# Optimization experiments

Hardware: AMD Instinct MI355X
Metric: run time of the kernel (lower is better)

## Reference

```python
import jax, jax.numpy as jnp
import numpy as np

N_NODES = 100000
N_EDGES = 3200000


def gcn_conv(x, src, dst, W, b, n):
    # GCNConv with self-loops and symmetric deg^-1/2 normalization (PyG defaults)
    loop = jnp.arange(n)
    s = jnp.concatenate([src, loop])
    d = jnp.concatenate([dst, loop])
    deg = jax.ops.segment_sum(jnp.ones_like(s, dtype=x.dtype), d, num_segments=n)
    dinv = jnp.where(deg > 0, jax.lax.rsqrt(deg), 0.0)
    norm = dinv[s] * dinv[d]                      # [E+N]
    h = x @ W.T                                   # [N, out]
    msgs = h[s] * norm[:, None]                   # gather + scale
    return jax.ops.segment_sum(msgs, d, num_segments=n) + b


def setup_inputs() -> dict:
    key = jax.random.key(0)
    k = jax.random.split(key, 6)
    x = jax.random.normal(k[0], (N_NODES, 64), dtype=jnp.float32)
    edge_index = jax.random.randint(k[1], (2, N_EDGES), 0, N_NODES, dtype=jnp.int64)
    # glorot-ish init for GCNConv linear weights, zero bias (PyG default bias init is zeros)
    W1 = jax.random.normal(k[2], (32, 64), dtype=jnp.float32) * (1.0 / np.sqrt(64))
    b1 = jnp.zeros((32,), dtype=jnp.float32)
    W2 = jax.random.normal(k[3], (16, 32), dtype=jnp.float32) * (1.0 / np.sqrt(32))
    b2 = jnp.zeros((16,), dtype=jnp.float32)
    return {"x": x, "edge_index": edge_index, "W1": W1, "b1": b1, "W2": W2, "b2": b2}


def reference(x, edge_index, W1, b1, W2, b2):
    n = x.shape[0]
    src, dst = edge_index[0], edge_index[1]
    # encode (eval mode: dropout is identity)
    h = jax.nn.relu(gcn_conv(x, src, dst, W1, b1, n))
    z = gcn_conv(h, src, dst, W2, b2, n)          # [N, 16]
    # decode: edge-wise dot product + sigmoid
    return jax.nn.sigmoid(jnp.sum(z[src] * z[dst], axis=-1))  # [E]
```

## Files before the change

kernel.cpp:

```cpp
#include <hip/hip_runtime.h>
#include <hip/hip_fp16.h>
#include <math.h>

#define NN 100000
#define NE 3200000
#define NB 391
#define NBH 256
#define CH 4096
#define NPART ((NE + CH - 1) / CH)

typedef unsigned long long u64;
typedef _Float16 h2 __attribute__((ext_vector_type(2)));

__device__ inline float2 u2f2(unsigned v) {
    __half2 h = *reinterpret_cast<__half2*>(&v);
    return __half22float2(h);
}

#if __has_builtin(__builtin_amdgcn_fdot2)
__device__ inline float dot2acc(unsigned a, unsigned b, float c) {
    union { unsigned u; h2 h; } ca, cb;
    ca.u = a; cb.u = b;
    return __builtin_amdgcn_fdot2(ca.h, cb.h, c, false);
}
#else
__device__ inline float dot2acc(unsigned a, unsigned b, float c) {
    float2 fa = u2f2(a), fb = u2f2(b);
    return c + fa.x * fb.x + fa.y * fb.y;
}
#endif

__global__ __launch_bounds__(256) void bhist_kernel(const int* __restrict__ dst,
                                                    int* __restrict__ part, int e) {
    __shared__ int h[NB];
    int tid = threadIdx.x;
    for (int i = tid; i < NB; i += 256) h[i] = 0;
    __syncthreads();
    for (int i = blockIdx.x * 256 + tid; i < e; i += NBH * 256)
        atomicAdd(&h[dst[i] >> 8], 1);
    __syncthreads();
    for (int i = tid; i < NB; i += 256)
        part[blockIdx.x * NB + i] = h[i];
}

__global__ __launch_bounds__(512) void bscan_kernel(const int* __restrict__ part,
                                                    int* __restrict__ bhist,
                                                    int* __restrict__ boffs,
                                                    int* __restrict__ cursor) {
    __shared__ int s[512];
    int tid = threadIdx.x;
    int v = 0;
    if (tid < NB) {
#pragma unroll 8
        for (int b = 0; b < NBH; ++b) v += part[b * NB + tid];
        bhist[tid] = v;
    }
    s[tid] = (tid < NB) ? v : 0;
    __syncthreads();
    for (int off = 1; off < 512; off <<= 1) {
        int t = (tid >= off) ? s[tid - off] : 0;
        __syncthreads();
        s[tid] += t;
        __syncthreads();
    }
    if (tid < NB) {
        int ex = s[tid] - v;
        boffs[tid] = ex;
        cursor[tid] = ex;
    }
}

__global__ __launch_bounds__(512) void partition_kernel(
        const int* __restrict__ src, const int* __restrict__ dst,
        int* __restrict__ cursor, int* __restrict__ adj, int e) {
    __shared__ int scnt[NB];
    __shared__ int sbase[NB];
    __shared__ int lexcl[NB];
    __shared__ int cur[NB];
    __shared__ int s[512];
    __shared__ int sdata[CH];

    int tid = threadIdx.x;
    int chunk0 = blockIdx.x * CH;

    for (int i = tid; i < NB; i += 512) scnt[i] = 0;
    __syncthreads();

#pragma unroll
    for (int k = 0; k < CH / 512; ++k) {
        int i = chunk0 + k * 512 + tid;
        if (i < e) atomicAdd(&scnt[dst[i] >> 8], 1);
    }
    __syncthreads();

    for (int b = tid; b < NB; b += 512)
        if (scnt[b]) sbase[b] = atomicAdd(&cursor[b], scnt[b]);

    s[tid] = (tid < NB) ? scnt[tid] : 0;
    __syncthreads();
    for (int off = 1; off < 512; off <<= 1) {
        int t = (tid >= off) ? s[tid - off] : 0;
        __syncthreads();
        s[tid] += t;
        __syncthreads();
    }
    if (tid < NB) {
        int ex = s[tid] - scnt[tid];
        lexcl[tid] = ex;
        cur[tid] = ex;
    }
    __syncthreads();

#pragma unroll
    for (int k = 0; k < CH / 512; ++k) {
        int i = chunk0 + k * 512 + tid;
        if (i < e) {
            int sv = src[i], d = dst[i];
            int b = d >> 8;
            int p = atomicAdd(&cur[b], 1);
            sdata[p] = (sv << 8) | (d & 255);
        }
    }
    __syncthreads();

    for (int b = tid; b < NB; b += 512) {
        int cb = scnt[b];
        if (cb) {
            int base = sbase[b];
            int start = lexcl[b];
            for (int k2 = 0; k2 < cb; ++k2)
                adj[base + k2] = sdata[start + k2];
        }
    }
}

__global__ __launch_bounds__(512) void csr_kernel(
        const int* __restrict__ bhist, const int* __restrict__ boffs,
        const int* __restrict__ adj, int* __restrict__ adj2,
        int* __restrict__ rowptr, float* __restrict__ dinv, int n) {
    __shared__ int cnt[256];
    __shared__ int s[256];
    __shared__ int cur[256];
    int tid = threadIdx.x;
    int b = blockIdx.x;
    if (tid < 256) cnt[tid] = 0;
    __syncthreads();
    int ebeg = boffs[b], ecnt = bhist[b];
    for (int j = tid; j < ecnt; j += 512)
        atomicAdd(&cnt[adj[ebeg + j] & 255], 1);
    __syncthreads();
    int v = 0;
    if (tid < 256) { v = cnt[tid]; s[tid] = v; }
    __syncthreads();
    for (int off = 1; off < 256; off <<= 1) {
        int t = 0;
        if (tid < 256 && tid >= off) t = s[tid - off];
        __syncthreads();
        if (tid < 256) s[tid] += t;
        __syncthreads();
    }
    if (tid < 256) {
        int excl = s[tid] - v;
        cur[tid] = excl;
        int node = b * 256 + tid;
        if (node < n) {
            rowptr[node] = ebeg + excl;
            dinv[node] = rsqrtf((float)v + 1.0f);
        }
        if (node == n) rowptr[n] = ebeg + excl;
    }
    __syncthreads();
    for (int j = tid; j < ecnt; j += 512) {
        int w = adj[ebeg + j];
        int p = atomicAdd(&cur[w & 255], 1);
        adj2[ebeg + p] = w >> 8;
    }
}

__global__ __launch_bounds__(256) void gemm1_kernel(
        const float* __restrict__ x, const float* __restrict__ W1,
        const float* __restrict__ dinv, __half* __restrict__ g1a,
        __half* __restrict__ g1b, int n) {
    __shared__ float sW[64 * 32];
    __shared__ float sX[32 * 65];
    int tid = threadIdx.x;
    for (int idx = tid; idx < 2048; idx += 256) {
        int k = idx >> 5, c = idx & 31;
        sW[idx] = W1[c * 64 + k];
    }
    int row0 = blockIdx.x * 32;
    for (int idx = tid; idx < 512; idx += 256) {
        int r = idx >> 4, q = idx & 15;
        int grow = row0 + r;
        float4 v = (grow < n) ? ((const float4*)x)[(size_t)grow * 16 + q]
                              : make_float4(0.f, 0.f, 0.f, 0.f);
        float* dp = &sX[r * 65 + q * 4];
        dp[0] = v.x; dp[1] = v.y; dp[2] = v.z; dp[3] = v.w;
    }
    __syncthreads();
    int r = tid >> 3, cg = tid & 7;
    const float4* sW4 = (const float4*)sW;
    float4 acc = make_float4(0.f, 0.f, 0.f, 0.f);
#pragma unroll
    for (int k = 0; k < 64; ++k) {
        float xk = sX[r * 65 + k];
        float4 w = sW4[k * 8 + cg];
        acc.x += xk * w.x; acc.y += xk * w.y; acc.z += xk * w.z; acc.w += xk * w.w;
    }
    int grow = row0 + r;
    if (grow < n) {
        float di = dinv[grow];
        __half2 h0 = __float22half2_rn(make_float2(acc.x * di, acc.y * di));
        __half2 h1 = __float22half2_rn(make_float2(acc.z * di, acc.w * di));
        uint2 packed;
        packed.x = *(unsigned*)&h0;
        packed.y = *(unsigned*)&h1;
        if (cg < 4) ((uint2*)g1a)[(size_t)grow * 4 + cg] = packed;
        else        ((uint2*)g1b)[(size_t)grow * 4 + (cg - 4)] = packed;
    }
}

__global__ __launch_bounds__(256) void agg1_kernel(
        const int* __restrict__ rowptr, const int* __restrict__ adj2,
        const float* __restrict__ dinv, const __half* __restrict__ gh,
        const float* __restrict__ b1, float* __restrict__ agg1, int n, int pass) {
    int t = blockIdx.x * blockDim.x + threadIdx.x;
    int node = t >> 3;
    if (node >= n) return;
    int c2 = t & 7;
    const unsigned* G = (const unsigned*)gh;
    float2 acc = u2f2(G[(size_t)node * 8 + c2]);
    int j = rowptr[node], end = rowptr[node + 1];
    for (; j + 7 < end; j += 8) {
        int s0 = adj2[j],     s1 = adj2[j + 1], s2 = adj2[j + 2], s3 = adj2[j + 3];
        int s4 = adj2[j + 4], s5 = adj2[j + 5], s6 = adj2[j + 6], s7 = adj2[j + 7];
        float2 v0 = u2f2(G[(size_t)s0 * 8 + c2]);
        float2 v1 = u2f2(G[(size_t)s1 * 8 + c2]);
        float2 v2 = u2f2(G[(size_t)s2 * 8 + c2]);
        float2 v3 = u2f2(G[(size_t)s3 * 8 + c2]);
        float2 v4 = u2f2(G[(size_t)s4 * 8 + c2]);
        float2 v5 = u2f2(G[(size_t)s5 * 8 + c2]);
        float2 v6 = u2f2(G[(size_t)s6 * 8 + c2]);
        float2 v7 = u2f2(G[(size_t)s7 * 8 + c2]);
        acc.x += ((v0.x + v1.x) + (v2.x + v3.x)) + ((v4.x + v5.x) + (v6.x + v7.x));
        acc.y += ((v0.y + v1.y) + (v2.y + v3.y)) + ((v4.y + v5.y) + (v6.y + v7.y));
    }
    for (; j + 3 < end; j += 4) {
        int s0 = adj2[j], s1 = adj2[j + 1], s2 = adj2[j + 2], s3 = adj2[j + 3];
        float2 v0 = u2f2(G[(size_t)s0 * 8 + c2]);
        float2 v1 = u2f2(G[(size_t)s1 * 8 + c2]);
        float2 v2 = u2f2(G[(size_t)s2 * 8 + c2]);
        float2 v3 = u2f2(G[(size_t)s3 * 8 + c2]);
        acc.x += (v0.x + v1.x) + (v2.x + v3.x);
        acc.y += (v0.y + v1.y) + (v2.y + v3.y);
    }
    for (; j < end; ++j) {
        float2 v = u2f2(G[(size_t)adj2[j] * 8 + c2]);
        acc.x += v.x; acc.y += v.y;
    }
    float di = dinv[node];
    float2 bb = ((const float2*)b1)[pass * 8 + c2];
    float2 outv = make_float2(bb.x + di * acc.x, bb.y + di * acc.y);
    ((float2*)agg1)[(size_t)node * 16 + pass * 8 + c2] = outv;
}

__global__ __launch_bounds__(256) void gemm2_kernel(
        const float* __restrict__ agg1, const float* __restrict__ W2,
        const float* __restrict__ dinv, __half* __restrict__ g2h, int n) {
    __shared__ float sW[32 * 16];
    __shared__ float sH[64 * 33];
    int tid = threadIdx.x;
    for (int idx = tid; idx < 512; idx += 256) {
        int k = idx >> 4, c = idx & 15;
        sW[idx] = W2[c * 32 + k];
    }
    int row0 = blockIdx.x * 64;
    for (int idx = tid; idx < 512; idx += 256) {
        int r = idx >> 3, q = idx & 7;
        int grow = row0 + r;
        float4 v = (grow < n) ? ((const float4*)agg1)[(size_t)grow * 8 + q]
                              : make_float4(0.f, 0.f, 0.f, 0.f);
        float* dp = &sH[r * 33 + q * 4];
        dp[0] = fmaxf(v.x, 0.f); dp[1] = fmaxf(v.y, 0.f);
        dp[2] = fmaxf(v.z, 0.f); dp[3] = fmaxf(v.w, 0.f);
    }
    __syncthreads();
    int r = tid >> 2, cg = tid & 3;
    const float4* sW4 = (const float4*)sW;
    float4 acc = make_float4(0.f, 0.f, 0.f, 0.f);
#pragma unroll
    for (int k = 0; k < 32; ++k) {
        float hk = sH[r * 33 + k];
        float4 w = sW4[k * 4 + cg];
        acc.x += hk * w.x; acc.y += hk * w.y; acc.z += hk * w.z; acc.w += hk * w.w;
    }
    int grow = row0 + r;
    if (grow < n) {
        float di = dinv[grow];
        __half2 h0 = __float22half2_rn(make_float2(acc.x * di, acc.y * di));
        __half2 h1 = __float22half2_rn(make_float2(acc.z * di, acc.w * di));
        uint2 packed;
        packed.x = *(unsigned*)&h0;
        packed.y = *(unsigned*)&h1;
        ((uint2*)g2h)[(size_t)grow * 4 + cg] = packed;
    }
}

__global__ __launch_bounds__(256) void agg2_kernel(
        const int* __restrict__ rowptr, const int* __restrict__ adj2,
        const float* __restrict__ dinv, const __half* __restrict__ g2h,
        const float* __restrict__ b2, __half* __restrict__ zh, int n) {
    int t = blockIdx.x * blockDim.x + threadIdx.x;
    int node = t >> 3;
    if (node >= n) return;
    int c2 = t & 7;
    const unsigned* G = (const unsigned*)g2h;
    float2 acc = u2f2(G[(size_t)node * 8 + c2]);
    int j = rowptr[node], end = rowptr[node + 1];
    for (; j + 7 < end; j += 8) {
        int s0 = adj2[j],     s1 = adj2[j + 1], s2 = adj2[j + 2], s3 = adj2[j + 3];
        int s4 = adj2[j + 4], s5 = adj2[j + 5], s6 = adj2[j + 6], s7 = adj2[j + 7];
        float2 v0 = u2f2(G[(size_t)s0 * 8 + c2]);
        float2 v1 = u2f2(G[(size_t)s1 * 8 + c2]);
        float2 v2 = u2f2(G[(size_t)s2 * 8 + c2]);
        float2 v3 = u2f2(G[(size_t)s3 * 8 + c2]);
        float2 v4 = u2f2(G[(size_t)s4 * 8 + c2]);
        float2 v5 = u2f2(G[(size_t)s5 * 8 + c2]);
        float2 v6 = u2f2(G[(size_t)s6 * 8 + c2]);
        float2 v7 = u2f2(G[(size_t)s7 * 8 + c2]);
        acc.x += ((v0.x + v1.x) + (v2.x + v3.x)) + ((v4.x + v5.x) + (v6.x + v7.x));
        acc.y += ((v0.y + v1.y) + (v2.y + v3.y)) + ((v4.y + v5.y) + (v6.y + v7.y));
    }
    for (; j + 3 < end; j += 4) {
        int s0 = adj2[j], s1 = adj2[j + 1], s2 = adj2[j + 2], s3 = adj2[j + 3];
        float2 v0 = u2f2(G[(size_t)s0 * 8 + c2]);
        float2 v1 = u2f2(G[(size_t)s1 * 8 + c2]);
        float2 v2 = u2f2(G[(size_t)s2 * 8 + c2]);
        float2 v3 = u2f2(G[(size_t)s3 * 8 + c2]);
        acc.x += (v0.x + v1.x) + (v2.x + v3.x);
        acc.y += (v0.y + v1.y) + (v2.y + v3.y);
    }
    for (; j < end; ++j) {
        float2 v = u2f2(G[(size_t)adj2[j] * 8 + c2]);
        acc.x += v.x; acc.y += v.y;
    }
    float di = dinv[node];
    float2 bb = ((const float2*)b2)[c2];
    __half2 outv = __float22half2_rn(make_float2(bb.x + di * acc.x, bb.y + di * acc.y));
    ((__half2*)zh)[(size_t)node * 8 + c2] = outv;
}

__global__ __launch_bounds__(256) void decode_kernel(
        const int* __restrict__ src, const int* __restrict__ dst,
        const __half* __restrict__ zh, float* __restrict__ out, int e) {
    int t = blockIdx.x * blockDim.x + threadIdx.x;
    int pair = t >> 1;
    int e0 = pair * 2;
    if (e0 >= e) return;
    int half = t & 1;
    u64 sv = *(const u64*)(src + e0);
    u64 dv = *(const u64*)(dst + e0);
    int s0 = (int)(unsigned)sv, s1 = (int)(sv >> 32);
    int d0 = (int)(unsigned)dv, d1 = (int)(dv >> 32);
    uint4 a0 = *((const uint4*)(zh + (size_t)s0 * 16) + half);
    uint4 b0 = *((const uint4*)(zh + (size_t)d0 * 16) + half);
    uint4 a1 = *((const uint4*)(zh + (size_t)s1 * 16) + half);
    uint4 b1 = *((const uint4*)(zh + (size_t)d1 * 16) + half);
    float p0 = 0.f, p1 = 0.f;
    p0 = dot2acc(a0.x, b0.x, p0); p0 = dot2acc(a0.y, b0.y, p0);
    p0 = dot2acc(a0.z, b0.z, p0); p0 = dot2acc(a0.w, b0.w, p0);
    p1 = dot2acc(a1.x, b1.x, p1); p1 = dot2acc(a1.y, b1.y, p1);
    p1 = dot2acc(a1.z, b1.z, p1); p1 = dot2acc(a1.w, b1.w, p1);
    float t0 = p0 + __shfl_xor(p0, 1, 64);
    float t1 = p1 + __shfl_xor(p1, 1, 64);
    if (half == 0) {
        float2 o;
        o.x = 1.0f / (1.0f + expf(-t0));
        o.y = 1.0f / (1.0f + expf(-t1));
        ((float2*)out)[pair] = o;
    }
}

extern "C" void kernel_launch(void* const* d_in, const int* in_sizes, int n_in,
                              void* d_out, int out_size, void* d_ws, size_t ws_size,
                              hipStream_t stream) {
    const float* x   = (const float*)d_in[0];
    const int* eidx  = (const int*)d_in[1];
    const float* W1  = (const float*)d_in[2];
    const float* b1  = (const float*)d_in[3];
    const float* W2  = (const float*)d_in[4];
    const float* b2  = (const float*)d_in[5];
    float* out = (float*)d_out;

    const int n = NN;
    const int e = NE;
    const int* src = eidx;
    const int* dst = eidx + e;

    int* bhist   = (int*)d_ws;
    int* boffs   = bhist + 512;
    int* cursor  = boffs + 512;
    int* rowptr  = cursor + 512;
    int* adj     = rowptr + 100004;
    int* adj2    = adj + e;
    float* dinv  = (float*)(adj2 + e);
    __half* g1a  = (__half*)adj;
    __half* g1b  = g1a + (size_t)n * 16;
    float* agg1  = dinv + n;
    __half* g2h  = (__half*)(agg1 + (size_t)n * 32);
    __half* zh   = g2h + (size_t)n * 16;
    int* part    = (int*)(zh + (size_t)n * 16);

    dim3 blk(256);

    bhist_kernel<<<NBH, blk, 0, stream>>>(dst, part, e);
    bscan_kernel<<<1, 512, 0, stream>>>(part, bhist, boffs, cursor);
    partition_kernel<<<NPART, 512, 0, stream>>>(src, dst, cursor, adj, e);
    csr_kernel<<<NB, 512, 0, stream>>>(bhist, boffs, adj, adj2, rowptr, dinv, n);

    gemm1_kernel<<<(n + 31) / 32, blk, 0, stream>>>(x, W1, dinv, g1a, g1b, n);
    agg1_kernel<<<(n * 8 + 255) / 256, blk, 0, stream>>>(rowptr, adj2, dinv, g1a, b1, agg1, n, 0);
    agg1_kernel<<<(n * 8 + 255) / 256, blk, 0, stream>>>(rowptr, adj2, dinv, g1b, b1, agg1, n, 1);

    gemm2_kernel<<<(n + 63) / 64, blk, 0, stream>>>(agg1, W2, dinv, g2h, n);
    agg2_kernel<<<(n * 8 + 255) / 256, blk, 0, stream>>>(rowptr, adj2, dinv, g2h, b2, zh, n);

    decode_kernel<<<(e + 255) / 256, blk, 0, stream>>>(src, dst, zh, out, e);
}
```

Measured before the change: 234.7 us.

## Aggregate with 4 lanes per node using 16-byte gathers and split edge lists

```diff
diff --git a/kernel.cpp b/kernel.cpp
--- a/kernel.cpp
+++ b/kernel.cpp
@@ -29,6 +29,14 @@
     return c + fa.x * fb.x + fa.y * fb.y;
 }
 #endif
+
+__device__ inline void acc8(float* a, uint4 v) {
+    float2 f;
+    f = u2f2(v.x); a[0] += f.x; a[1] += f.y;
+    f = u2f2(v.y); a[2] += f.x; a[3] += f.y;
+    f = u2f2(v.z); a[4] += f.x; a[5] += f.y;
+    f = u2f2(v.w); a[6] += f.x; a[7] += f.y;
+}
 
 __global__ __launch_bounds__(256) void bhist_kernel(const int* __restrict__ dst,
                                                     int* __restrict__ part, int e) {
@@ -225,43 +233,57 @@
         const float* __restrict__ dinv, const __half* __restrict__ gh,
         const float* __restrict__ b1, float* __restrict__ agg1, int n, int pass) {
     int t = blockIdx.x * blockDim.x + threadIdx.x;
-    int node = t >> 3;
+    int node = t >> 2;
     if (node >= n) return;
-    int c2 = t & 7;
-    const unsigned* G = (const unsigned*)gh;
-    float2 acc = u2f2(G[(size_t)node * 8 + c2]);
-    int j = rowptr[node], end = rowptr[node + 1];
-    for (; j + 7 < end; j += 8) {
+    int sub = t & 3;
+    int slice = sub >> 1, ch = sub & 1;
+    const uint4* G = (const uint4*)gh;
+    float acc[8] = {0.f, 0.f, 0.f, 0.f, 0.f, 0.f, 0.f, 0.f};
+    if (slice == 0)
+        acc8(acc, G[(size_t)node * 2 + ch]);
+    int beg = rowptr[node], end = rowptr[node + 1];
+    int deg = end - beg;
+    int half0 = (deg + 1) >> 1;
+    int j    = beg + slice * half0;
+    int jend = slice ? end : beg + half0;
+    for (; j + 7 < jend; j += 8) {
         int s0 = adj2[j],     s1 = adj2[j + 1], s2 = adj2[j + 2], s3 = adj2[j + 3];
         int s4 = adj2[j + 4], s5 = adj2[j + 5], s6 = adj2[j + 6], s7 = adj2[j + 7];
-        float2 v0 = u2f2(G[(size_t)s0 * 8 + c2]);
-        float2 v1 = u2f2(G[(size_t)s1 * 8 + c2]);
-        float2 v2 = u2f2(G[(size_t)s2 * 8 + c2]);
-        float2 v3 = u2f2(G[(size_t)s3 * 8 + c2]);
-        float2 v4 = u2f2(G[(size_t)s4 * 8 + c2]);
-        float2 v5 = u2f2(G[(size_t)s5 * 8 + c2]);
-        float2 v6 = u2f2(G[(size_t)s6 * 8 + c2]);
-        float2 v7 = u2f2(G[(size_t)s7 * 8 + c2]);
-        acc.x += ((v0.x + v1.x) + (v2.x + v3.x)) + ((v4.x + v5.x) + (v6.x + v7.x));
-        acc.y += ((v0.y + v1.y) + (v2.y + v3.y)) + ((v4.y + v5.y) + (v6.y + v7.y));
-    }
-    for (; j + 3 < end; j += 4) {
+        uint4 v0 = G[(size_t)s0 * 2 + ch];
+        uint4 v1 = G[(size_t)s1 * 2 + ch];
+        uint4 v2 = G[(size_t)s2 * 2 + ch];
+        uint4 v3 = G[(size_t)s3 * 2 + ch];
+        uint4 v4 = G[(size_t)s4 * 2 + ch];
+        uint4 v5 = G[(size_t)s5 * 2 + ch];
+        uint4 v6 = G[(size_t)s6 * 2 + ch];
+        uint4 v7 = G[(size_t)s7 * 2 + ch];
+        acc8(acc, v0); acc8(acc, v1); acc8(acc, v2); acc8(acc, v3);
+        acc8(acc, v4); acc8(acc, v5); acc8(acc, v6); acc8(acc, v7);
+    }
+    for (; j + 3 < jend; j += 4) {
         int s0 = adj2[j], s1 = adj2[j + 1], s2 = adj2[j + 2], s3 = adj2[j + 3];
-        float2 v0 = u2f2(G[(size_t)s0 * 8 + c2]);
-        float2 v1 = u2f2(G[(size_t)s1 * 8 + c2]);
-        float2 v2 = u2f2(G[(size_t)s2 * 8 + c2]);
-        float2 v3 = u2f2(G[(size_t)s3 * 8 + c2]);
-        acc.x += (v0.x + v1.x) + (v2.x + v3.x);
-        acc.y += (v0.y + v1.y) + (v2.y + v3.y);
-    }
-    for (; j < end; ++j) {
-        float2 v = u2f2(G[(size_t)adj2[j] * 8 + c2]);
-        acc.x += v.x; acc.y += v.y;
-    }
-    float di = dinv[node];
-    float2 bb = ((const float2*)b1)[pass * 8 + c2];
-    float2 outv = make_float2(bb.x + di * acc.x, bb.y + di * acc.y);
-    ((float2*)agg1)[(size_t)node * 16 + pass * 8 + c2] = outv;
+        uint4 v0 = G[(size_t)s0 * 2 + ch];
+        uint4 v1 = G[(size_t)s1 * 2 + ch];
+        uint4 v2 = G[(size_t)s2 * 2 + ch];
+        uint4 v3 = G[(size_t)s3 * 2 + ch];
+        acc8(acc, v0); acc8(acc, v1); acc8(acc, v2); acc8(acc, v3);
+    }
+    for (; j < jend; ++j)
+        acc8(acc, G[(size_t)adj2[j] * 2 + ch]);
+#pragma unroll
+    for (int k = 0; k < 8; ++k)
+        acc[k] += __shfl_xor(acc[k], 2, 64);
+    if (slice == 0) {
+        float di = dinv[node];
+        float4 bb0 = ((const float4*)b1)[pass * 4 + ch * 2];
+        float4 bb1 = ((const float4*)b1)[pass * 4 + ch * 2 + 1];
+        float4 o0 = make_float4(bb0.x + di * acc[0], bb0.y + di * acc[1],
+                                bb0.z + di * acc[2], bb0.w + di * acc[3]);
+        float4 o1 = make_float4(bb1.x + di * acc[4], bb1.y + di * acc[5],
+                                bb1.z + di * acc[6], bb1.w + di * acc[7]);
+        ((float4*)agg1)[(size_t)node * 8 + pass * 4 + ch * 2]     = o0;
+        ((float4*)agg1)[(size_t)node * 8 + pass * 4 + ch * 2 + 1] = o1;
+    }
 }
 
 __global__ __launch_bounds__(256) void gemm2_kernel(
@@ -311,43 +333,59 @@
         const float* __restrict__ dinv, const __half* __restrict__ g2h,
         const float* __restrict__ b2, __half* __restrict__ zh, int n) {
     int t = blockIdx.x * blockDim.x + threadIdx.x;
-    int node = t >> 3;
+    int node = t >> 2;
     if (node >= n) return;
-    int c2 = t & 7;
-    const unsigned* G = (const unsigned*)g2h;
-    float2 acc = u2f2(G[(size_t)node * 8 + c2]);
-    int j = rowptr[node], end = rowptr[node + 1];
-    for (; j + 7 < end; j += 8) {
+    int sub = t & 3;
+    int slice = sub >> 1, ch = sub & 1;
+    const uint4* G = (const uint4*)g2h;
+    float acc[8] = {0.f, 0.f, 0.f, 0.f, 0.f, 0.f, 0.f, 0.f};
+    if (slice == 0)
+        acc8(acc, G[(size_t)node * 2 + ch]);
+    int beg = rowptr[node], end = rowptr[node + 1];
+    int deg = end - beg;
+    int half0 = (deg + 1) >> 1;
+    int j    = beg + slice * half0;
+    int jend = slice ? end : beg + half0;
+    for (; j + 7 < jend; j += 8) {
         int s0 = adj2[j],     s1 = adj2[j + 1], s2 = adj2[j + 2], s3 = adj2[j + 3];
         int s4 = adj2[j + 4], s5 = adj2[j + 5], s6 = adj2[j + 6], s7 = adj2[j + 7];
-        float2 v0 = u2f2(G[(size_t)s0 * 8 + c2]);
-        float2 v1 = u2f2(G[(size_t)s1 * 8 + c2]);
-        float2 v2 = u2f2(G[(size_t)s2 * 8 + c2]);
-        float2 v3 = u2f2(G[(size_t)s3 * 8 + c2]);
-        float2 v4 = u2f2(G[(size_t)s4 * 8 + c2]);
-        float2 v5 = u2f2(G[(size_t)s5 * 8 + c2]);
-        float2 v6 = u2f2(G[(size_t)s6 * 8 + c2]);
-        float2 v7 = u2f2(G[(size_t)s7 * 8 + c2]);
-        acc.x += ((v0.x + v1.x) + (v2.x + v3.x)) + ((v4.x + v5.x) + (v6.x + v7.x));
-        acc.y += ((v0.y + v1.y) + (v2.y + v3.y)) + ((v4.y + v5.y) + (v6.y + v7.y));
-    }
-    for (; j + 3 < end; j += 4) {
+        uint4 v0 = G[(size_t)s0 * 2 + ch];
+        uint4 v1 = G[(size_t)s1 * 2 + ch];
+        uint4 v2 = G[(size_t)s2 * 2 + ch];
+        uint4 v3 = G[(size_t)s3 * 2 + ch];
+        uint4 v4 = G[(size_t)s4 * 2 + ch];
+        uint4 v5 = G[(size_t)s5 * 2 + ch];
+        uint4 v6 = G[(size_t)s6 * 2 + ch];
+        uint4 v7 = G[(size_t)s7 * 2 + ch];
+        acc8(acc, v0); acc8(acc, v1); acc8(acc, v2); acc8(acc, v3);
+        acc8(acc, v4); acc8(acc, v5); acc8(acc, v6); acc8(acc, v7);
+    }
+    for (; j + 3 < jend; j += 4) {
         int s0 = adj2[j], s1 = adj2[j + 1], s2 = adj2[j + 2], s3 = adj2[j + 3];
-        float2 v0 = u2f2(G[(size_t)s0 * 8 + c2]);
-        float2 v1 = u2f2(G[(size_t)s1 * 8 + c2]);
-        float2 v2 = u2f2(G[(size_t)s2 * 8 + c2]);
-        float2 v3 = u2f2(G[(size_t)s3 * 8 + c2]);
-        acc.x += (v0.x + v1.x) + (v2.x + v3.x);
-        acc.y += (v0.y + v1.y) + (v2.y + v3.y);
-    }
-    for (; j < end; ++j) {
-        float2 v = u2f2(G[(size_t)adj2[j] * 8 + c2]);
-        acc.x += v.x; acc.y += v.y;
-    }
-    float di = dinv[node];
-    float2 bb = ((const float2*)b2)[c2];
-    __half2 outv = __float22half2_rn(make_float2(bb.x + di * acc.x, bb.y + di * acc.y));
-    ((__half2*)zh)[(size_t)node * 8 + c2] = outv;
+        uint4 v0 = G[(size_t)s0 * 2 + ch];
+        uint4 v1 = G[(size_t)s1 * 2 + ch];
+        uint4 v2 = G[(size_t)s2 * 2 + ch];
+        uint4 v3 = G[(size_t)s3 * 2 + ch];
+        acc8(acc, v0); acc8(acc, v1); acc8(acc, v2); acc8(acc, v3);
+    }
+    for (; j < jend; ++j)
+        acc8(acc, G[(size_t)adj2[j] * 2 + ch]);
+#pragma unroll
+    for (int k = 0; k < 8; ++k)
+        acc[k] += __shfl_xor(acc[k], 2, 64);
+    if (slice == 0) {
+        float di = dinv[node];
+        float4 bb0 = ((const float4*)b2)[ch * 2];
+        float4 bb1 = ((const float4*)b2)[ch * 2 + 1];
+        __half2 p0 = __float22half2_rn(make_float2(bb0.x + di * acc[0], bb0.y + di * acc[1]));
+        __half2 p1 = __float22half2_rn(make_float2(bb0.z + di * acc[2], bb0.w + di * acc[3]));
+        __half2 p2 = __float22half2_rn(make_float2(bb1.x + di * acc[4], bb1.y + di * acc[5]));
+        __half2 p3 = __float22half2_rn(make_float2(bb1.z + di * acc[6], bb1.w + di * acc[7]));
+        uint4 packed;
+        packed.x = *(unsigned*)&p0; packed.y = *(unsigned*)&p1;
+        packed.z = *(unsigned*)&p2; packed.w = *(unsigned*)&p3;
+        ((uint4*)zh)[(size_t)node * 2 + ch] = packed;
+    }
 }
 
 __global__ __launch_bounds__(256) void decode_kernel(
@@ -419,11 +457,11 @@
     csr_kernel<<<NB, 512, 0, stream>>>(bhist, boffs, adj, adj2, rowptr, dinv, n);
 
     gemm1_kernel<<<(n + 31) / 32, blk, 0, stream>>>(x, W1, dinv, g1a, g1b, n);
-    agg1_kernel<<<(n * 8 + 255) / 256, blk, 0, stream>>>(rowptr, adj2, dinv, g1a, b1, agg1, n, 0);
-    agg1_kernel<<<(n * 8 + 255) / 256, blk, 0, stream>>>(rowptr, adj2, dinv, g1b, b1, agg1, n, 1);
+    agg1_kernel<<<(n * 4 + 255) / 256, blk, 0, stream>>>(rowptr, adj2, dinv, g1a, b1, agg1, n, 0);
+    agg1_kernel<<<(n * 4 + 255) / 256, blk, 0, stream>>>(rowptr, adj2, dinv, g1b, b1, agg1, n, 1);
 
     gemm2_kernel<<<(n + 63) / 64, blk, 0, stream>>>(agg1, W2, dinv, g2h, n);
-    agg2_kernel<<<(n * 8 + 255) / 256, blk, 0, stream>>>(rowptr, adj2, dinv, g2h, b2, zh, n);
+    agg2_kernel<<<(n * 4 + 255) / 256, blk, 0, stream>>>(rowptr, adj2, dinv, g2h, b2, zh, n);
 
     decode_kernel<<<(e + 255) / 256, blk, 0, stream>>>(src, dst, zh, out, e);
 }
```

Result: no change. 235.4 us (+0.3%).
